# Kernel optimization log

Hardware: AMD Instinct MI355X
Metric: run time of the kernel (lower is better)

Reference implementation:

```python
import jax, jax.numpy as jnp
import numpy as np

NUM_HEADS = 8

def setup_inputs() -> dict:
    key = jax.random.key(0)
    k1, k2, k3, k4 = jax.random.split(key, 4)
    B, N, S, C = 16, 256, 4096, 512
    return {
        "query": jax.random.normal(k1, (B, N, C), dtype=jnp.float32),
        "key": jax.random.normal(k2, (B, S, C), dtype=jnp.float32),
        "Wq": jax.random.normal(k3, (C, C), dtype=jnp.float32) * (C ** -0.5),
        "Wk": jax.random.normal(k4, (C, C), dtype=jnp.float32) * (C ** -0.5),
    }

def reference(query, key, Wq, Wk):
    B, N, C = query.shape
    S = key.shape[1]
    H = NUM_HEADS
    hd = C // H
    scale = hd ** -0.5
    # value = key (v_proj is Identity, value defaults to key)
    q = (query @ Wq).reshape(B, N, H, hd)   # b n h c
    k = (key @ Wk).reshape(B, S, H, hd)     # b s h c
    raw_attn = jnp.einsum('bnhc,bshc->bhns', q, k) * scale  # [B,H,N,S]
    # softmax over the QUERY axis (dim=-2), non-standard
    attn = jax.nn.softmax(raw_attn, axis=-2)
    # clamp-normalize over token axis; divisor is detached in the original
    div = jnp.clip(jnp.sum(attn, axis=-1, keepdims=True), 1.0, None)
    attn = attn / jax.lax.stop_gradient(div)
    # attn_drop has p=0.0 -> identity
    v = key.reshape(B, S, H, hd)
    out = jnp.einsum('bhns,bshc->bnhc', attn, v).reshape(B, N, C)
    # out_style = attn @ key_heads; since value == key this equals out
    out_style = out
    return out, out_style
```

## Files before the change

### kernel.cpp

```cpp
#include <hip/hip_runtime.h>
#include <hip/hip_bf16.h>


typedef __attribute__((ext_vector_type(8))) short bf16x8;
typedef __attribute__((ext_vector_type(4))) float f32x4;
typedef unsigned int u32;

__device__ __forceinline__ unsigned short f2bf(float f) {
  union { __hip_bfloat16 h; unsigned short u; } cv;
  cv.h = __float2bfloat16(f);
  return cv.u;
}

__device__ __forceinline__ void async_copy16(const void* gptr, void* lptr) {
  __builtin_amdgcn_global_load_lds((const __attribute__((address_space(1))) u32*)gptr,
                                   (__attribute__((address_space(3))) u32*)lptr,
                                   16, 0, 0);
}

__global__ __launch_bounds__(256) void prep_w(const float* __restrict__ Wq,
                                              const float* __restrict__ Wk,
                                              unsigned short* __restrict__ WtQ,
                                              unsigned short* __restrict__ WtK) {
  __shared__ float tile[64][65];
  const int blk = blockIdx.x;
  const float* W = (blk & 1) ? Wk : Wq;
  unsigned short* Wt = (blk & 1) ? WtK : WtQ;
  const int tb = blk >> 1;
  const int k0 = (tb >> 3) * 64, n0 = (tb & 7) * 64;
  const int t = threadIdx.x;
  const int row = t >> 4, col4 = (t & 15) * 4;
#pragma unroll
  for (int i = 0; i < 4; ++i) {
    int r = i * 16 + row;
    float4 v = *reinterpret_cast<const float4*>(&W[(size_t)(k0 + r) * 512 + n0 + col4]);
    tile[r][col4 + 0] = v.x; tile[r][col4 + 1] = v.y;
    tile[r][col4 + 2] = v.z; tile[r][col4 + 3] = v.w;
  }
  __syncthreads();
#pragma unroll
  for (int i = 0; i < 4; ++i) {
    int r = i * 16 + row;
    short4 s;
    s.x = (short)f2bf(tile[col4 + 0][r]);
    s.y = (short)f2bf(tile[col4 + 1][r]);
    s.z = (short)f2bf(tile[col4 + 2][r]);
    s.w = (short)f2bf(tile[col4 + 3][r]);
    *reinterpret_cast<short4*>(&Wt[(size_t)(n0 + r) * 512 + k0 + col4]) = s;
  }
}

__global__ __launch_bounds__(256, 3) void gemm_xw(const float* __restrict__ X,
                                                  const unsigned short* __restrict__ Wt,
                                                  __hip_bfloat16* __restrict__ Y) {
  __shared__ float As[128 * 64];
  __shared__ unsigned short Bs[128 * 64];
  const int t = threadIdx.x;
  const int wave = t >> 6, lane = t & 63, l15 = lane & 15, quad = lane >> 4;
  const int n0 = blockIdx.x * 128, m0 = blockIdx.y * 128;
  const int wm = (wave >> 1) * 64, wn = (wave & 1) * 64;

  const int a_rl = lane >> 4;
  const int b_rl = lane >> 3;
  const int b_cs = (lane & 7) ^ b_rl;

  f32x4 acc[4][4];
#pragma unroll
  for (int i = 0; i < 4; ++i)
#pragma unroll
    for (int j = 0; j < 4; ++j) { f32x4 z = {0.f, 0.f, 0.f, 0.f}; acc[i][j] = z; }

  for (int k0 = 0; k0 < 512; k0 += 64) {
    __syncthreads();
    {
      const float* aBase = X + (size_t)m0 * 512 + k0;
#pragma unroll
      for (int o = 0; o < 8; ++o) {
        int rg = wave * 8 + o;
        int r = rg * 4 + a_rl;
        int cs = (lane & 15) ^ (r & 7);
        async_copy16(aBase + (size_t)r * 512 + cs * 4, &As[rg * 256]);
      }
      const unsigned short* bBase = Wt + (size_t)n0 * 512 + k0;
#pragma unroll
      for (int o = 0; o < 4; ++o) {
        int rg = wave * 4 + o;
        int r = rg * 8 + b_rl;
        async_copy16(bBase + (size_t)r * 512 + b_cs * 8, &Bs[rg * 512]);
      }
    }
    __syncthreads();

#pragma unroll
    for (int x = 0; x < 2; ++x) {
      bf16x8 a[4], bfr[4];
#pragma unroll
      for (int i = 0; i < 4; ++i) {
        int ra = wm + 16 * i + l15;
        int c0 = x * 8 + quad * 2;
        float4 f0 = *reinterpret_cast<const float4*>(&As[(ra * 16 + (c0 ^ (ra & 7))) * 4]);
        float4 f1 = *reinterpret_cast<const float4*>(&As[(ra * 16 + ((c0 + 1) ^ (ra & 7))) * 4]);
        union { bf16x8 v; unsigned short s[8]; } u;
        u.s[0] = f2bf(f0.x); u.s[1] = f2bf(f0.y); u.s[2] = f2bf(f0.z); u.s[3] = f2bf(f0.w);
        u.s[4] = f2bf(f1.x); u.s[5] = f2bf(f1.y); u.s[6] = f2bf(f1.z); u.s[7] = f2bf(f1.w);
        a[i] = u.v;
      }
#pragma unroll
      for (int j = 0; j < 4; ++j) {
        int rb = wn + 16 * j + l15;
        int cb = x * 4 + quad;
        bfr[j] = *reinterpret_cast<const bf16x8*>(&Bs[(rb * 8 + (cb ^ (rb & 7))) * 8]);
      }
#pragma unroll
      for (int i = 0; i < 4; ++i)
#pragma unroll
        for (int j = 0; j < 4; ++j)
          acc[i][j] = __builtin_amdgcn_mfma_f32_16x16x32_bf16(a[i], bfr[j], acc[i][j], 0, 0, 0);
    }
  }
#pragma unroll
  for (int i = 0; i < 4; ++i)
#pragma unroll
    for (int j = 0; j < 4; ++j)
#pragma unroll
      for (int r = 0; r < 4; ++r) {
        int m = m0 + wm + 16 * i + 4 * quad + r;
        int n = n0 + wn + 16 * j + l15;
        Y[(size_t)m * 512 + n] = __float2bfloat16(acc[i][j][r]);
      }
}

__global__ __launch_bounds__(512, 2) void attn_kernel(const __hip_bfloat16* __restrict__ qg,
                                                      const __hip_bfloat16* __restrict__ kg,
                                                      const float* __restrict__ keyg,
                                                      float* __restrict__ accg,
                                                      float* __restrict__ rsg) {
  __shared__ unsigned short ks[64][72];
  __shared__ unsigned short vs[64][66];
  __shared__ unsigned short ps[256][72];
  __shared__ float red[8][64];

  const int t = threadIdx.x;
  const int wave = t >> 6, lane = t & 63, l15 = lane & 15, quad = lane >> 4;
  const int blk = blockIdx.x, chunk = blk & 1, bh = blk >> 1, b = bh >> 3, h = bh & 7;

  bf16x8 qf[2][2];
#pragma unroll
  for (int i = 0; i < 2; ++i)
#pragma unroll
    for (int x = 0; x < 2; ++x) {
      const unsigned short* p = (const unsigned short*)qg +
          (size_t)(b * 256 + wave * 32 + 16 * i + l15) * 512 + h * 64 + x * 32 + quad * 8;
      qf[i][x] = *reinterpret_cast<const bf16x8*>(p);
    }

  union { bf16x8 f; int w[4]; } ones_u;
  ones_u.w[0] = 0x3F803F80; ones_u.w[1] = 0x3F803F80;
  ones_u.w[2] = 0x3F803F80; ones_u.w[3] = 0x3F803F80;
  const bf16x8 ones = ones_u.f;

  f32x4 oacc[2][4], rsacc[2];
#pragma unroll
  for (int i = 0; i < 2; ++i) {
    f32x4 z = {0.f, 0.f, 0.f, 0.f};
    rsacc[i] = z;
#pragma unroll
    for (int j = 0; j < 4; ++j) oacc[i][j] = z;
  }

  const int s0base = chunk * 2048;
  for (int it = 0; it < 32; ++it) {
    const int s0 = s0base + it * 64;
    __syncthreads();
    {
      const unsigned short* kbase = (const unsigned short*)kg + ((size_t)(b * 4096 + s0)) * 512 + h * 64;
#pragma unroll
      for (int i = 0; i < 2; ++i) {
        int lin = i * 512 + t, row = lin >> 4, c4 = (lin & 15) << 2;
        *reinterpret_cast<short4*>(&ks[row][c4]) =
            *reinterpret_cast<const short4*>(kbase + (size_t)row * 512 + c4);
      }
      const float* vbase = keyg + ((size_t)(b * 4096 + s0)) * 512 + h * 64;
#pragma unroll
      for (int i = 0; i < 2; ++i) {
        int lin = i * 512 + t, row = lin >> 4, c4 = (lin & 15) << 2;
        int sig = 4 * (row & 15) + (row >> 4);
        float4 v = *reinterpret_cast<const float4*>(vbase + (size_t)row * 512 + c4);
        vs[c4 + 0][sig] = f2bf(v.x);
        vs[c4 + 1][sig] = f2bf(v.y);
        vs[c4 + 2][sig] = f2bf(v.z);
        vs[c4 + 3][sig] = f2bf(v.w);
      }
    }
    __syncthreads();

    f32x4 L[2][4];
#pragma unroll
    for (int i = 0; i < 2; ++i)
#pragma unroll
      for (int j = 0; j < 4; ++j) { f32x4 z = {0.f, 0.f, 0.f, 0.f}; L[i][j] = z; }
#pragma unroll
    for (int x = 0; x < 2; ++x) {
      bf16x8 bfr[4];
#pragma unroll
      for (int j = 0; j < 4; ++j)
        bfr[j] = *reinterpret_cast<const bf16x8*>(&ks[16 * j + l15][x * 32 + quad * 8]);
#pragma unroll
      for (int i = 0; i < 2; ++i)
#pragma unroll
        for (int j = 0; j < 4; ++j)
          L[i][j] = __builtin_amdgcn_mfma_f32_16x16x32_bf16(qf[i][x], bfr[j], L[i][j], 0, 0, 0);
    }

    float csum[4] = {0.f, 0.f, 0.f, 0.f};
#pragma unroll
    for (int i = 0; i < 2; ++i)
#pragma unroll
      for (int j = 0; j < 4; ++j)
#pragma unroll
        for (int r = 0; r < 4; ++r) {
          float e = __expf(L[i][j][r] * 0.125f);
          L[i][j][r] = e;
          csum[j] += e;
        }
#pragma unroll
    for (int j = 0; j < 4; ++j) {
      float v = csum[j];
      v += __shfl_xor(v, 16);
      v += __shfl_xor(v, 32);
      csum[j] = v;
    }
    if (quad == 0) {
#pragma unroll
      for (int j = 0; j < 4; ++j) red[wave][16 * j + l15] = csum[j];
    }
    __syncthreads();
    float rcol[4];
#pragma unroll
    for (int j = 0; j < 4; ++j) {
      int s = 16 * j + l15;
      rcol[j] = 1.0f / (red[0][s] + red[1][s] + red[2][s] + red[3][s] +
                        red[4][s] + red[5][s] + red[6][s] + red[7][s]);
    }

#pragma unroll
    for (int i = 0; i < 2; ++i)
#pragma unroll
      for (int r = 0; r < 4; ++r) {
        int nloc = wave * 32 + 16 * i + 4 * quad + r;
        short4 s4;
        s4.x = (short)f2bf(L[i][0][r] * rcol[0]);
        s4.y = (short)f2bf(L[i][1][r] * rcol[1]);
        s4.z = (short)f2bf(L[i][2][r] * rcol[2]);
        s4.w = (short)f2bf(L[i][3][r] * rcol[3]);
        *reinterpret_cast<short4*>(&ps[nloc][4 * l15]) = s4;
      }

#pragma unroll
    for (int x = 0; x < 2; ++x) {
      bf16x8 ap[2], bv[4];
#pragma unroll
      for (int i = 0; i < 2; ++i)
        ap[i] = *reinterpret_cast<const bf16x8*>(&ps[wave * 32 + 16 * i + l15][x * 32 + quad * 8]);
#pragma unroll
      for (int j = 0; j < 4; ++j) {
        const int* vp = reinterpret_cast<const int*>(&vs[16 * j + l15][x * 32 + quad * 8]);
        union { bf16x8 f; int w[4]; } u;
        u.w[0] = vp[0]; u.w[1] = vp[1]; u.w[2] = vp[2]; u.w[3] = vp[3];
        bv[j] = u.f;
      }
#pragma unroll
      for (int i = 0; i < 2; ++i) {
#pragma unroll
        for (int j = 0; j < 4; ++j)
          oacc[i][j] = __builtin_amdgcn_mfma_f32_16x16x32_bf16(ap[i], bv[j], oacc[i][j], 0, 0, 0);
        rsacc[i] = __builtin_amdgcn_mfma_f32_16x16x32_bf16(ap[i], ones, rsacc[i], 0, 0, 0);
      }
    }
  }

  float* rsp = rsg + chunk * 32768 + bh * 256;
  if (l15 == 0) {
#pragma unroll
    for (int i = 0; i < 2; ++i)
#pragma unroll
      for (int r = 0; r < 4; ++r)
        rsp[wave * 32 + 16 * i + 4 * quad + r] = rsacc[i][r];
  }
  float* ap_ = accg + (size_t)chunk * 2097152 + (size_t)bh * 16384;
#pragma unroll
  for (int i = 0; i < 2; ++i)
#pragma unroll
    for (int j = 0; j < 4; ++j)
#pragma unroll
      for (int r = 0; r < 4; ++r)
        ap_[(wave * 32 + 16 * i + 4 * quad + r) * 64 + 16 * j + l15] = oacc[i][j][r];
}

__global__ __launch_bounds__(256) void finalize(const float* __restrict__ acc,
                                                const float* __restrict__ rs,
                                                float* __restrict__ out) {
  int idx = blockIdx.x * 256 + threadIdx.x;
  int c = idx & 63, n = (idx >> 6) & 255, bh = idx >> 14;
  float v = acc[idx] + acc[idx + 2097152];
  float r = rs[bh * 256 + n] + rs[32768 + bh * 256 + n];
  float o = v / fmaxf(r, 1.0f);
  int b = bh >> 3, h = bh & 7;
  size_t oi = ((size_t)(b * 256 + n)) * 512 + h * 64 + c;
  out[oi] = o;
  out[oi + 2097152] = o;
}

extern "C" void kernel_launch(void* const* d_in, const int* in_sizes, int n_in,
                              void* d_out, int out_size, void* d_ws, size_t ws_size,
                              hipStream_t stream) {
  const float* query = (const float*)d_in[0];
  const float* key   = (const float*)d_in[1];
  const float* Wq    = (const float*)d_in[2];
  const float* Wk    = (const float*)d_in[3];
  float* out = (float*)d_out;
  char* ws = (char*)d_ws;

  unsigned short* WtQ = (unsigned short*)(ws);
  unsigned short* WtK = (unsigned short*)(ws + 524288);
  __hip_bfloat16* qbf = (__hip_bfloat16*)(ws + 1048576);
  __hip_bfloat16* kbf = (__hip_bfloat16*)(ws + 5242880);
  float* accw = (float*)(ws + 72351744);
  float* rsw  = (float*)(ws + 89128960);

  prep_w<<<128, 256, 0, stream>>>(Wq, Wk, WtQ, WtK);
  gemm_xw<<<dim3(4, 32), 256, 0, stream>>>(query, WtQ, qbf);
  gemm_xw<<<dim3(4, 512), 256, 0, stream>>>(key, WtK, kbf);
  attn_kernel<<<256, 512, 0, stream>>>(qbf, kbf, key, accw, rsw);
  finalize<<<8192, 256, 0, stream>>>(accw, rsw, out);
}
```

Before: 354.3 us.

## Split attention over four key chunks with atomic reduction and async swizzled K loads

Raises the key-axis split from two to four chunks, giving 512 blocks instead of 256 to fill more CUs. Partial outputs and row sums are accumulated with float atomics into a zero-initialised workspace, so finalize reads one buffer. K tiles are loaded with direct global-to-LDS async copies into an XOR-swizzled layout, V is transposed with packed bf16 stores, and P stores use packed conversion. This adds a memset, atomic contention, and a higher occupancy target that may pressure registers.

```diff
diff --git a/kernel.cpp b/kernel.cpp
--- a/kernel.cpp
+++ b/kernel.cpp
@@ -9,6 +9,12 @@
 __device__ __forceinline__ unsigned short f2bf(float f) {
   union { __hip_bfloat16 h; unsigned short u; } cv;
   cv.h = __float2bfloat16(f);
+  return cv.u;
+}
+
+__device__ __forceinline__ u32 pkbf(float a, float b) {
+  union { __hip_bfloat162 h; u32 u; } cv;
+  cv.h = __float22bfloat162_rn(float2{a, b});
   return cv.u;
 }
 
@@ -130,19 +136,19 @@
       }
 }
 
-__global__ __launch_bounds__(512, 2) void attn_kernel(const __hip_bfloat16* __restrict__ qg,
+__global__ __launch_bounds__(512, 4) void attn_kernel(const __hip_bfloat16* __restrict__ qg,
                                                       const __hip_bfloat16* __restrict__ kg,
                                                       const float* __restrict__ keyg,
                                                       float* __restrict__ accg,
                                                       float* __restrict__ rsg) {
-  __shared__ unsigned short ks[64][72];
+  __shared__ unsigned short ks[64 * 64];
   __shared__ unsigned short vs[64][66];
   __shared__ unsigned short ps[256][72];
   __shared__ float red[8][64];
 
   const int t = threadIdx.x;
   const int wave = t >> 6, lane = t & 63, l15 = lane & 15, quad = lane >> 4;
-  const int blk = blockIdx.x, chunk = blk & 1, bh = blk >> 1, b = bh >> 3, h = bh & 7;
+  const int blk = blockIdx.x, chunk = blk & 3, bh = blk >> 2, b = bh >> 3, h = bh & 7;
 
   bf16x8 qf[2][2];
 #pragma unroll
@@ -168,28 +174,26 @@
     for (int j = 0; j < 4; ++j) oacc[i][j] = z;
   }
 
-  const int s0base = chunk * 2048;
-  for (int it = 0; it < 32; ++it) {
+  const int s0base = chunk * 1024;
+  const int krow = lane >> 3, kchunk = (lane & 7) ^ krow;
+  for (int it = 0; it < 16; ++it) {
     const int s0 = s0base + it * 64;
     __syncthreads();
     {
       const unsigned short* kbase = (const unsigned short*)kg + ((size_t)(b * 4096 + s0)) * 512 + h * 64;
-#pragma unroll
-      for (int i = 0; i < 2; ++i) {
-        int lin = i * 512 + t, row = lin >> 4, c4 = (lin & 15) << 2;
-        *reinterpret_cast<short4*>(&ks[row][c4]) =
-            *reinterpret_cast<const short4*>(kbase + (size_t)row * 512 + c4);
-      }
+      async_copy16(kbase + (size_t)(wave * 8 + krow) * 512 + kchunk * 8, &ks[wave * 512]);
+
       const float* vbase = keyg + ((size_t)(b * 4096 + s0)) * 512 + h * 64;
-#pragma unroll
-      for (int i = 0; i < 2; ++i) {
-        int lin = i * 512 + t, row = lin >> 4, c4 = (lin & 15) << 2;
-        int sig = 4 * (row & 15) + (row >> 4);
-        float4 v = *reinterpret_cast<const float4*>(vbase + (size_t)row * 512 + c4);
-        vs[c4 + 0][sig] = f2bf(v.x);
-        vs[c4 + 1][sig] = f2bf(v.y);
-        vs[c4 + 2][sig] = f2bf(v.z);
-        vs[c4 + 3][sig] = f2bf(v.w);
+      const int c = lane;
+#pragma unroll
+      for (int kk = 0; kk < 2; ++kk) {
+        int k2 = wave + 8 * kk;
+#pragma unroll
+        for (int p = 0; p < 2; ++p) {
+          float va = vbase[(size_t)(32 * p + k2) * 512 + c];
+          float vb = vbase[(size_t)(32 * p + 16 + k2) * 512 + c];
+          *reinterpret_cast<u32*>(&vs[c][4 * k2 + 2 * p]) = pkbf(va, vb);
+        }
       }
     }
     __syncthreads();
@@ -203,8 +207,11 @@
     for (int x = 0; x < 2; ++x) {
       bf16x8 bfr[4];
 #pragma unroll
-      for (int j = 0; j < 4; ++j)
-        bfr[j] = *reinterpret_cast<const bf16x8*>(&ks[16 * j + l15][x * 32 + quad * 8]);
+      for (int j = 0; j < 4; ++j) {
+        int rb = 16 * j + l15;
+        int phys = (x * 4 + quad) ^ (rb & 7);
+        bfr[j] = *reinterpret_cast<const bf16x8*>(&ks[rb * 64 + phys * 8]);
+      }
 #pragma unroll
       for (int i = 0; i < 2; ++i)
 #pragma unroll
@@ -248,12 +255,10 @@
 #pragma unroll
       for (int r = 0; r < 4; ++r) {
         int nloc = wave * 32 + 16 * i + 4 * quad + r;
-        short4 s4;
-        s4.x = (short)f2bf(L[i][0][r] * rcol[0]);
-        s4.y = (short)f2bf(L[i][1][r] * rcol[1]);
-        s4.z = (short)f2bf(L[i][2][r] * rcol[2]);
-        s4.w = (short)f2bf(L[i][3][r] * rcol[3]);
-        *reinterpret_cast<short4*>(&ps[nloc][4 * l15]) = s4;
+        u32 w0 = pkbf(L[i][0][r] * rcol[0], L[i][1][r] * rcol[1]);
+        u32 w1 = pkbf(L[i][2][r] * rcol[2], L[i][3][r] * rcol[3]);
+        u32* dst = reinterpret_cast<u32*>(&ps[nloc][4 * l15]);
+        dst[0] = w0; dst[1] = w1;
       }
 
 #pragma unroll
@@ -279,22 +284,23 @@
     }
   }
 
-  float* rsp = rsg + chunk * 32768 + bh * 256;
+  float* rsp = rsg + bh * 256;
   if (l15 == 0) {
 #pragma unroll
     for (int i = 0; i < 2; ++i)
 #pragma unroll
       for (int r = 0; r < 4; ++r)
-        rsp[wave * 32 + 16 * i + 4 * quad + r] = rsacc[i][r];
-  }
-  float* ap_ = accg + (size_t)chunk * 2097152 + (size_t)bh * 16384;
+        unsafeAtomicAdd(&rsp[wave * 32 + 16 * i + 4 * quad + r], rsacc[i][r]);
+  }
+  float* ap_ = accg + (size_t)bh * 16384;
 #pragma unroll
   for (int i = 0; i < 2; ++i)
 #pragma unroll
     for (int j = 0; j < 4; ++j)
 #pragma unroll
       for (int r = 0; r < 4; ++r)
-        ap_[(wave * 32 + 16 * i + 4 * quad + r) * 64 + 16 * j + l15] = oacc[i][j][r];
+        unsafeAtomicAdd(&ap_[(wave * 32 + 16 * i + 4 * quad + r) * 64 + 16 * j + l15],
+                        oacc[i][j][r]);
 }
 
 __global__ __launch_bounds__(256) void finalize(const float* __restrict__ acc,
@@ -302,8 +308,8 @@
                                                 float* __restrict__ out) {
   int idx = blockIdx.x * 256 + threadIdx.x;
   int c = idx & 63, n = (idx >> 6) & 255, bh = idx >> 14;
-  float v = acc[idx] + acc[idx + 2097152];
-  float r = rs[bh * 256 + n] + rs[32768 + bh * 256 + n];
+  float v = acc[idx];
+  float r = rs[bh * 256 + n];
   float o = v / fmaxf(r, 1.0f);
   int b = bh >> 3, h = bh & 7;
   size_t oi = ((size_t)(b * 256 + n)) * 512 + h * 64 + c;
@@ -326,11 +332,12 @@
   __hip_bfloat16* qbf = (__hip_bfloat16*)(ws + 1048576);
   __hip_bfloat16* kbf = (__hip_bfloat16*)(ws + 5242880);
   float* accw = (float*)(ws + 72351744);
-  float* rsw  = (float*)(ws + 89128960);
+  float* rsw  = (float*)(ws + 80740352);
 
   prep_w<<<128, 256, 0, stream>>>(Wq, Wk, WtQ, WtK);
   gemm_xw<<<dim3(4, 32), 256, 0, stream>>>(query, WtQ, qbf);
   gemm_xw<<<dim3(4, 512), 256, 0, stream>>>(key, WtK, kbf);
-  attn_kernel<<<256, 512, 0, stream>>>(qbf, kbf, key, accw, rsw);
+  hipMemsetAsync(ws + 72351744, 0, 8519680, stream);
+  attn_kernel<<<512, 512, 0, stream>>>(qbf, kbf, key, accw, rsw);
   finalize<<<8192, 256, 0, stream>>>(accw, rsw, out);
 }
```

Measured after the change: 382.5 us. 1.08x slower.

## Restructure attention loop: keys-major QK tiles, register prefetch, swizzled LDS, 128-key steps

Applied to the files above, without the earlier changes.

Stages the whole Q head tile in XOR-swizzled LDS and lets each wave own 16 keys, computing S^T so the softmax over queries reduces within a wave via shuffles. This removes the cross-wave shared-memory reduction and one barrier per step. The key step grows to 128, and the next K fragments and V rows are prefetched into registers during the current step, overlapping global loads with MFMA work. The cost is heavier register pressure (16 accumulator tiles plus prefetch buffers) and a larger LDS footprint, which may lower occupancy.

```diff
diff --git a/kernel.cpp b/kernel.cpp
--- a/kernel.cpp
+++ b/kernel.cpp
@@ -9,6 +9,12 @@
 __device__ __forceinline__ unsigned short f2bf(float f) {
   union { __hip_bfloat16 h; unsigned short u; } cv;
   cv.h = __float2bfloat16(f);
+  return cv.u;
+}
+
+__device__ __forceinline__ u32 pkbf(float a, float b) {
+  union { __hip_bfloat162 h; u32 u; } cv;
+  cv.h = __float22bfloat162_rn(float2{a, b});
   return cv.u;
 }
 
@@ -135,24 +141,39 @@
                                                       const float* __restrict__ keyg,
                                                       float* __restrict__ accg,
                                                       float* __restrict__ rsg) {
-  __shared__ unsigned short ks[64][72];
-  __shared__ unsigned short vs[64][66];
-  __shared__ unsigned short ps[256][72];
-  __shared__ float red[8][64];
+  __shared__ unsigned short qs[256 * 64];
+  __shared__ unsigned short vs[64 * 128];
+  __shared__ unsigned short pst[256 * 128];
 
   const int t = threadIdx.x;
   const int wave = t >> 6, lane = t & 63, l15 = lane & 15, quad = lane >> 4;
   const int blk = blockIdx.x, chunk = blk & 1, bh = blk >> 1, b = bh >> 3, h = bh & 7;
-
-  bf16x8 qf[2][2];
-#pragma unroll
-  for (int i = 0; i < 2; ++i)
-#pragma unroll
-    for (int x = 0; x < 2; ++x) {
-      const unsigned short* p = (const unsigned short*)qg +
-          (size_t)(b * 256 + wave * 32 + 16 * i + l15) * 512 + h * 64 + x * 32 + quad * 8;
-      qf[i][x] = *reinterpret_cast<const bf16x8*>(p);
-    }
+  const int l7 = l15 & 7;
+
+  {
+    const unsigned short* qbase = (const unsigned short*)qg + (size_t)(b * 256) * 512 + h * 64;
+#pragma unroll
+    for (int i = 0; i < 4; ++i) {
+      int lin = i * 512 + t;
+      int n = lin >> 3, cc = lin & 7, phys = cc ^ (n & 7);
+      bf16x8 v = *reinterpret_cast<const bf16x8*>(qbase + (size_t)n * 512 + cc * 8);
+      *reinterpret_cast<bf16x8*>(&qs[n * 64 + phys * 8]) = v;
+    }
+  }
+
+  const unsigned short* kbase = (const unsigned short*)kg + (size_t)(b * 4096 + chunk * 2048) * 512 + h * 64;
+  const float* vbase = keyg + (size_t)(b * 4096 + chunk * 2048) * 512 + h * 64;
+
+  bf16x8 kc0 = *reinterpret_cast<const bf16x8*>(kbase + (size_t)(16 * wave + l15) * 512 + quad * 8);
+  bf16x8 kc1 = *reinterpret_cast<const bf16x8*>(kbase + (size_t)(16 * wave + l15) * 512 + 32 + quad * 8);
+  float vbuf[16];
+#pragma unroll
+  for (int half = 0; half < 2; ++half) {
+    int sc = wave + 8 * half;
+#pragma unroll
+    for (int j = 0; j < 8; ++j)
+      vbuf[half * 8 + j] = vbase[(size_t)(sc * 8 + j) * 512 + lane];
+  }
 
   union { bf16x8 f; int w[4]; } ones_u;
   ones_u.w[0] = 0x3F803F80; ones_u.w[1] = 0x3F803F80;
@@ -168,113 +189,98 @@
     for (int j = 0; j < 4; ++j) oacc[i][j] = z;
   }
 
-  const int s0base = chunk * 2048;
-  for (int it = 0; it < 32; ++it) {
-    const int s0 = s0base + it * 64;
+  __syncthreads();
+
+  for (int it = 0; it < 16; ++it) {
+    f32x4 L[16];
+#pragma unroll
+    for (int jt = 0; jt < 16; ++jt) { f32x4 z = {0.f, 0.f, 0.f, 0.f}; L[jt] = z; }
+#pragma unroll
+    for (int x = 0; x < 2; ++x) {
+      bf16x8 kf = x ? kc1 : kc0;
+#pragma unroll
+      for (int jt = 0; jt < 16; ++jt) {
+        bf16x8 bq = *reinterpret_cast<const bf16x8*>(
+            &qs[(16 * jt + l15) * 64 + ((4 * x + quad) ^ l7) * 8]);
+        L[jt] = __builtin_amdgcn_mfma_f32_16x16x32_bf16(kf, bq, L[jt], 0, 0, 0);
+      }
+    }
+
+    const int nit = (it < 15) ? it + 1 : 15;
+    kc0 = *reinterpret_cast<const bf16x8*>(kbase + (size_t)(nit * 128 + 16 * wave + l15) * 512 + quad * 8);
+    kc1 = *reinterpret_cast<const bf16x8*>(kbase + (size_t)(nit * 128 + 16 * wave + l15) * 512 + 32 + quad * 8);
+
+    float cs0 = 0.f, cs1 = 0.f, cs2 = 0.f, cs3 = 0.f;
+#pragma unroll
+    for (int jt = 0; jt < 16; ++jt) {
+      float e0 = __expf(L[jt][0] * 0.125f);
+      float e1 = __expf(L[jt][1] * 0.125f);
+      float e2 = __expf(L[jt][2] * 0.125f);
+      float e3 = __expf(L[jt][3] * 0.125f);
+      L[jt][0] = e0; L[jt][1] = e1; L[jt][2] = e2; L[jt][3] = e3;
+      cs0 += e0; cs1 += e1; cs2 += e2; cs3 += e3;
+    }
+#pragma unroll
+    for (int m = 1; m <= 8; m <<= 1) {
+      cs0 += __shfl_xor(cs0, m);
+      cs1 += __shfl_xor(cs1, m);
+      cs2 += __shfl_xor(cs2, m);
+      cs3 += __shfl_xor(cs3, m);
+    }
+    const float ri0 = 1.0f / cs0, ri1 = 1.0f / cs1, ri2 = 1.0f / cs2, ri3 = 1.0f / cs3;
+
     __syncthreads();
+
+#pragma unroll
+    for (int half = 0; half < 2; ++half) {
+      int sc = wave + 8 * half;
+      uint4 w;
+      w.x = pkbf(vbuf[half * 8 + 0], vbuf[half * 8 + 1]);
+      w.y = pkbf(vbuf[half * 8 + 2], vbuf[half * 8 + 3]);
+      w.z = pkbf(vbuf[half * 8 + 4], vbuf[half * 8 + 5]);
+      w.w = pkbf(vbuf[half * 8 + 6], vbuf[half * 8 + 7]);
+      *reinterpret_cast<uint4*>(&vs[lane * 128 + (sc ^ (lane & 7)) * 8]) = w;
+    }
+
     {
-      const unsigned short* kbase = (const unsigned short*)kg + ((size_t)(b * 4096 + s0)) * 512 + h * 64;
-#pragma unroll
-      for (int i = 0; i < 2; ++i) {
-        int lin = i * 512 + t, row = lin >> 4, c4 = (lin & 15) << 2;
-        *reinterpret_cast<short4*>(&ks[row][c4]) =
-            *reinterpret_cast<const short4*>(kbase + (size_t)row * 512 + c4);
-      }
-      const float* vbase = keyg + ((size_t)(b * 4096 + s0)) * 512 + h * 64;
-#pragma unroll
-      for (int i = 0; i < 2; ++i) {
-        int lin = i * 512 + t, row = lin >> 4, c4 = (lin & 15) << 2;
-        int sig = 4 * (row & 15) + (row >> 4);
-        float4 v = *reinterpret_cast<const float4*>(vbase + (size_t)row * 512 + c4);
-        vs[c4 + 0][sig] = f2bf(v.x);
-        vs[c4 + 1][sig] = f2bf(v.y);
-        vs[c4 + 2][sig] = f2bf(v.z);
-        vs[c4 + 3][sig] = f2bf(v.w);
-      }
-    }
+      const int scw = 2 * wave + (quad >> 1);
+      const int half8 = (quad & 1) * 4;
+#pragma unroll
+      for (int jt = 0; jt < 16; ++jt) {
+        uint2 w;
+        w.x = pkbf(L[jt][0] * ri0, L[jt][1] * ri1);
+        w.y = pkbf(L[jt][2] * ri2, L[jt][3] * ri3);
+        int row = 16 * jt + l15;
+        *reinterpret_cast<uint2*>(&pst[row * 128 + ((scw ^ l7) * 8) + half8]) = w;
+      }
+    }
+
     __syncthreads();
 
-    f32x4 L[2][4];
-#pragma unroll
-    for (int i = 0; i < 2; ++i)
-#pragma unroll
-      for (int j = 0; j < 4; ++j) { f32x4 z = {0.f, 0.f, 0.f, 0.f}; L[i][j] = z; }
-#pragma unroll
-    for (int x = 0; x < 2; ++x) {
-      bf16x8 bfr[4];
-#pragma unroll
-      for (int j = 0; j < 4; ++j)
-        bfr[j] = *reinterpret_cast<const bf16x8*>(&ks[16 * j + l15][x * 32 + quad * 8]);
-#pragma unroll
-      for (int i = 0; i < 2; ++i)
-#pragma unroll
-        for (int j = 0; j < 4; ++j)
-          L[i][j] = __builtin_amdgcn_mfma_f32_16x16x32_bf16(qf[i][x], bfr[j], L[i][j], 0, 0, 0);
-    }
-
-    float csum[4] = {0.f, 0.f, 0.f, 0.f};
-#pragma unroll
-    for (int i = 0; i < 2; ++i)
-#pragma unroll
-      for (int j = 0; j < 4; ++j)
-#pragma unroll
-        for (int r = 0; r < 4; ++r) {
-          float e = __expf(L[i][j][r] * 0.125f);
-          L[i][j][r] = e;
-          csum[j] += e;
-        }
-#pragma unroll
-    for (int j = 0; j < 4; ++j) {
-      float v = csum[j];
-      v += __shfl_xor(v, 16);
-      v += __shfl_xor(v, 32);
-      csum[j] = v;
-    }
-    if (quad == 0) {
-#pragma unroll
-      for (int j = 0; j < 4; ++j) red[wave][16 * j + l15] = csum[j];
-    }
-    __syncthreads();
-    float rcol[4];
-#pragma unroll
-    for (int j = 0; j < 4; ++j) {
-      int s = 16 * j + l15;
-      rcol[j] = 1.0f / (red[0][s] + red[1][s] + red[2][s] + red[3][s] +
-                        red[4][s] + red[5][s] + red[6][s] + red[7][s]);
-    }
-
-#pragma unroll
-    for (int i = 0; i < 2; ++i)
-#pragma unroll
-      for (int r = 0; r < 4; ++r) {
-        int nloc = wave * 32 + 16 * i + 4 * quad + r;
-        short4 s4;
-        s4.x = (short)f2bf(L[i][0][r] * rcol[0]);
-        s4.y = (short)f2bf(L[i][1][r] * rcol[1]);
-        s4.z = (short)f2bf(L[i][2][r] * rcol[2]);
-        s4.w = (short)f2bf(L[i][3][r] * rcol[3]);
-        *reinterpret_cast<short4*>(&ps[nloc][4 * l15]) = s4;
-      }
-
-#pragma unroll
-    for (int x = 0; x < 2; ++x) {
-      bf16x8 ap[2], bv[4];
-#pragma unroll
-      for (int i = 0; i < 2; ++i)
-        ap[i] = *reinterpret_cast<const bf16x8*>(&ps[wave * 32 + 16 * i + l15][x * 32 + quad * 8]);
-#pragma unroll
-      for (int j = 0; j < 4; ++j) {
-        const int* vp = reinterpret_cast<const int*>(&vs[16 * j + l15][x * 32 + quad * 8]);
-        union { bf16x8 f; int w[4]; } u;
-        u.w[0] = vp[0]; u.w[1] = vp[1]; u.w[2] = vp[2]; u.w[3] = vp[3];
-        bv[j] = u.f;
-      }
-#pragma unroll
-      for (int i = 0; i < 2; ++i) {
-#pragma unroll
-        for (int j = 0; j < 4; ++j)
-          oacc[i][j] = __builtin_amdgcn_mfma_f32_16x16x32_bf16(ap[i], bv[j], oacc[i][j], 0, 0, 0);
-        rsacc[i] = __builtin_amdgcn_mfma_f32_16x16x32_bf16(ap[i], ones, rsacc[i], 0, 0, 0);
+#pragma unroll
+    for (int half = 0; half < 2; ++half) {
+      int sc = wave + 8 * half;
+#pragma unroll
+      for (int j = 0; j < 8; ++j)
+        vbuf[half * 8 + j] = vbase[(size_t)(nit * 128 + sc * 8 + j) * 512 + lane];
+    }
+
+#pragma unroll
+    for (int kc = 0; kc < 4; ++kc) {
+      bf16x8 bv[4];
+#pragma unroll
+      for (int jc = 0; jc < 4; ++jc)
+        bv[jc] = *reinterpret_cast<const bf16x8*>(
+            &vs[(16 * jc + l15) * 128 + ((4 * kc + quad) ^ l7) * 8]);
+#pragma unroll
+      for (int jtl = 0; jtl < 2; ++jtl) {
+        int rowp = 16 * (2 * wave + jtl) + l15;
+        bf16x8 ap = *reinterpret_cast<const bf16x8*>(
+            &pst[rowp * 128 + ((4 * kc + quad) ^ l7) * 8]);
+#pragma unroll
+        for (int jc = 0; jc < 4; ++jc)
+          oacc[jtl][jc] = __builtin_amdgcn_mfma_f32_16x16x32_bf16(ap, bv[jc], oacc[jtl][jc], 0, 0, 0);
+        rsacc[jtl] = __builtin_amdgcn_mfma_f32_16x16x32_bf16(ap, ones, rsacc[jtl], 0, 0, 0);
       }
     }
   }
@@ -282,19 +288,19 @@
   float* rsp = rsg + chunk * 32768 + bh * 256;
   if (l15 == 0) {
 #pragma unroll
-    for (int i = 0; i < 2; ++i)
+    for (int jtl = 0; jtl < 2; ++jtl)
 #pragma unroll
       for (int r = 0; r < 4; ++r)
-        rsp[wave * 32 + 16 * i + 4 * quad + r] = rsacc[i][r];
+        rsp[16 * (2 * wave + jtl) + 4 * quad + r] = rsacc[jtl][r];
   }
   float* ap_ = accg + (size_t)chunk * 2097152 + (size_t)bh * 16384;
 #pragma unroll
-  for (int i = 0; i < 2; ++i)
-#pragma unroll
-    for (int j = 0; j < 4; ++j)
+  for (int jtl = 0; jtl < 2; ++jtl)
+#pragma unroll
+    for (int jc = 0; jc < 4; ++jc)
 #pragma unroll
       for (int r = 0; r < 4; ++r)
-        ap_[(wave * 32 + 16 * i + 4 * quad + r) * 64 + 16 * j + l15] = oacc[i][j][r];
+        ap_[(16 * (2 * wave + jtl) + 4 * quad + r) * 64 + 16 * jc + l15] = oacc[jtl][jc][r];
 }
 
 __global__ __launch_bounds__(256) void finalize(const float* __restrict__ acc,
```

New measurement: 333.5 us. 5.9% less time.
